# Kernel optimization log

Measured on AMD Instinct MI355X. Metric: run time of the kernel, lower is better.

Reference implementation:

```python
import jax, jax.numpy as jnp
import numpy as np

H = 384  # LSTM hidden size


def _conv1d(x, w, b, stride):
    # x: [B, T, Cin], w: [K, Cin, Cout] (flax 'SAME' padding, channels-last)
    y = jax.lax.conv_general_dilated(
        x, w, window_strides=(stride,), padding='SAME',
        dimension_numbers=('NWC', 'WIO', 'NWC'))
    return y + b


def _lstm(x, Wi, Wh, b, reverse):
    # x: [B, T, D]; Wi: [D, 4H] (input proj, no bias in flax LSTMCell input dense),
    # Wh: [H, 4H] (recurrent proj), b: [4H]. Gate order: i, f, g, o.
    if reverse:
        x = x[:, ::-1]
    B = x.shape[0]
    # precompute all input-to-gate projections in one big GEMM: [B, T, 4H]
    xg = jnp.einsum('btd,dh->bth', x, Wi)

    def step(carry, xg_t):
        c, h = carry
        z = xg_t + h @ Wh + b                      # [B, 4H]
        i, f, g, o = jnp.split(z, 4, axis=-1)
        i = jax.nn.sigmoid(i)
        f = jax.nn.sigmoid(f)
        g = jnp.tanh(g)
        o = jax.nn.sigmoid(o)
        c = f * c + i * g
        h = o * jnp.tanh(c)
        return (c, h), h

    init = (jnp.zeros((B, H), x.dtype), jnp.zeros((B, H), x.dtype))
    _, hs = jax.lax.scan(step, init, jnp.swapaxes(xg, 0, 1))  # hs: [T, B, H]
    hs = jnp.swapaxes(hs, 0, 1)
    if reverse:  # keep_order=True: flip output back to original time order
        hs = hs[:, ::-1]
    return hs


def setup_inputs() -> dict:
    key = jax.random.key(0)
    ks = jax.random.split(key, 12)
    s = 0.05
    B, T = 128, 8000
    return {
        'x': jax.random.normal(ks[0], (B, T, 1), jnp.float32),
        'conv1_w': jax.random.normal(ks[1], (5, 1, 4), jnp.float32) * s,
        'conv1_b': jnp.zeros((4,), jnp.float32),
        'conv2_w': jax.random.normal(ks[2], (5, 4, 16), jnp.float32) * s,
        'conv2_b': jnp.zeros((16,), jnp.float32),
        'conv3_w': jax.random.normal(ks[3], (19, 16, H), jnp.float32) * s,
        'conv3_b': jnp.zeros((H,), jnp.float32),
        'lstm_Wi': jax.random.normal(ks[4], (5, H, 4 * H), jnp.float32) * s,
        'lstm_Wh': jax.random.normal(ks[5], (5, H, 4 * H), jnp.float32) * s,
        'lstm_b': jnp.zeros((5, 4 * H), jnp.float32),
        'dense_w': jax.random.normal(ks[6], (H, 5), jnp.float32) * s,
        'dense_b': jnp.zeros((5,), jnp.float32),
    }


def reference(x, conv1_w, conv1_b, conv2_w, conv2_b, conv3_w, conv3_b,
              lstm_Wi, lstm_Wh, lstm_b, dense_w, dense_b):
    # CNN feature extractor
    x = jax.nn.silu(_conv1d(x, conv1_w, conv1_b, 1))
    x = jax.nn.silu(_conv1d(x, conv2_w, conv2_b, 1))
    x = jax.nn.silu(_conv1d(x, conv3_w, conv3_b, 5))   # [B, T/5, 384]
    # 5 stacked LSTMs, layers 1,3,5 reversed (keep_order), layers 2,4 forward
    for i in range(5):
        x = _lstm(x, lstm_Wi[i], lstm_Wh[i], lstm_b[i], reverse=(i % 2 == 0))
    # CTC head
    return x @ dense_w + dense_b                       # [B, T/5, 5]
```

## Files before the change

kernel.cpp:

```cpp
#include <hip/hip_runtime.h>
#include <math.h>

#define B_SZ 128
#define T_IN 8000
#define T_OUT 1600
#define HDIM 384
#define GDIM 1536
#define TC 40
#define NCHUNK (T_OUT / TC)
#define NTILES (12 * (B_SZ * TC / 128))
#define NLB 64

typedef _Float16 f16;
typedef __attribute__((ext_vector_type(2))) _Float16 f16x2;
typedef __attribute__((ext_vector_type(4))) _Float16 f16x4;
typedef __attribute__((ext_vector_type(8))) _Float16 f16x8;
typedef __attribute__((ext_vector_type(4))) float f32x4;
typedef __attribute__((ext_vector_type(4))) unsigned int u32x4;

__device__ inline float fdot2(f16x2 a, f16x2 b, float c) {
#if __has_builtin(__builtin_amdgcn_fdot2)
  return __builtin_amdgcn_fdot2(a, b, c, false);
#else
  return fmaf((float)a[0], (float)b[0], fmaf((float)a[1], (float)b[1], c));
#endif
}

__device__ inline float rcp_fast(float x) {
#if __has_builtin(__builtin_amdgcn_rcpf)
  return __builtin_amdgcn_rcpf(x);
#else
  return 1.f / x;
#endif
}
__device__ inline float sigf(float z) { return rcp_fast(1.f + __expf(-z)); }
__device__ inline float tanh_fast(float z) {
  z = fminf(fmaxf(z, -15.f), 15.f);
  float e = __expf(2.f * z);
  return (e - 1.f) * rcp_fast(e + 1.f);
}

__global__ __launch_bounds__(256) void conv12_kernel(
    const float* __restrict__ x, const float* __restrict__ w1, const float* __restrict__ b1,
    const float* __restrict__ w2, const float* __restrict__ b2, f16* __restrict__ y2) {
  __shared__ float sw1[20], sb1[4], sw2[320], sb2[16];
  int tid = threadIdx.x;
  if (tid < 20) sw1[tid] = w1[tid];
  if (tid < 4)  sb1[tid] = b1[tid];
  if (tid < 16) sb2[tid] = b2[tid];
  for (int i = tid; i < 320; i += 256) sw2[i] = w2[i];
  __syncthreads();
  int flat = blockIdx.x * 256 + tid;
  int b = flat / T_IN, t = flat % T_IN;
  const float* xb = x + (size_t)b * T_IN;
  float xv[9];
#pragma unroll
  for (int d = 0; d < 9; ++d) {
    int tt = t + d - 4;
    xv[d] = (tt >= 0 && tt < T_IN) ? xb[tt] : 0.f;
  }
  float y1[5][4];
#pragma unroll
  for (int u = 0; u < 5; ++u) {
    int tau = t + u - 2;
    bool valid = (tau >= 0 && tau < T_IN);
#pragma unroll
    for (int co = 0; co < 4; ++co) {
      float a = sb1[co];
#pragma unroll
      for (int k = 0; k < 5; ++k) a = fmaf(xv[u + k], sw1[k * 4 + co], a);
      y1[u][co] = valid ? (a / (1.f + expf(-a))) : 0.f;
    }
  }
  f16x8 o0, o1;
#pragma unroll
  for (int co = 0; co < 16; ++co) {
    float a = sb2[co];
#pragma unroll
    for (int u = 0; u < 5; ++u)
#pragma unroll
      for (int ci = 0; ci < 4; ++ci)
        a = fmaf(y1[u][ci], sw2[(u * 4 + ci) * 16 + co], a);
    float sv = a / (1.f + expf(-a));
    if (co < 8) o0[co] = (f16)sv; else o1[co - 8] = (f16)sv;
  }
  f16x8* dst = (f16x8*)(y2 + (size_t)flat * 16);
  dst[0] = o0;
  dst[1] = o1;
}

__global__ __launch_bounds__(384) void conv3_kernel(
    const f16* __restrict__ y2, const float* __restrict__ w3, const float* __restrict__ b3,
    f16* __restrict__ act) {
  __shared__ float in_s[94 * 16];
  int tid = threadIdx.x;
  int b = blockIdx.y;
  int t0 = blockIdx.x * 16;
  int base_t = t0 * 5 - 7;
  for (int i = tid; i < 94 * 16; i += 384) {
    int tau = i >> 4, ci = i & 15;
    int tt = base_t + tau;
    in_s[i] = (tt >= 0 && tt < T_IN) ? (float)y2[((size_t)b * T_IN + tt) * 16 + ci] : 0.f;
  }
  __syncthreads();
  int c = tid;
  float acc[16];
  float bv = b3[c];
#pragma unroll
  for (int tt = 0; tt < 16; ++tt) acc[tt] = bv;
  for (int kk = 0; kk < 19; ++kk) {
#pragma unroll
    for (int c4 = 0; c4 < 4; ++c4) {
      float wa = w3[(size_t)((kk * 16 + c4 * 4 + 0) * 384) + c];
      float wb = w3[(size_t)((kk * 16 + c4 * 4 + 1) * 384) + c];
      float wc = w3[(size_t)((kk * 16 + c4 * 4 + 2) * 384) + c];
      float wd = w3[(size_t)((kk * 16 + c4 * 4 + 3) * 384) + c];
#pragma unroll
      for (int tt = 0; tt < 16; ++tt) {
        const float4 iv = *(const float4*)&in_s[(tt * 5 + kk) * 16 + c4 * 4];
        acc[tt] = fmaf(iv.x, wa, acc[tt]);
        acc[tt] = fmaf(iv.y, wb, acc[tt]);
        acc[tt] = fmaf(iv.z, wc, acc[tt]);
        acc[tt] = fmaf(iv.w, wd, acc[tt]);
      }
    }
  }
#pragma unroll
  for (int tt = 0; tt < 16; ++tt) {
    float a = acc[tt];
    a = a / (1.f + expf(-a));
    act[((size_t)b * T_OUT + t0 + tt) * HDIM + c] = (f16)a;
  }
}

__global__ __launch_bounds__(256) void whcvt_kernel(
    const float* __restrict__ Wh, f16x2* __restrict__ whB) {
  size_t idx = (size_t)blockIdx.x * 256 + threadIdx.x;
  int d = (int)(idx & 3);
  size_t r1 = idx >> 2;
  int lane = (int)(r1 & 63);
  size_t r2 = r1 >> 6;
  int ks = (int)(r2 % 12);
  size_t r3 = r2 / 12;
  int nt = (int)(r3 % 12);
  size_t r4 = r3 / 12;
  int isl = (int)(r4 & 7);
  int L = (int)(r4 >> 3);
  int cz = nt * 16 + (lane & 15);
  int gate = cz & 3;
  int jj = cz >> 2;
  int gcol = gate * 384 + isl * 48 + jj;
  int k2d = ks * 16 + (lane >> 4) * 4 + d;
  const float* src = Wh + ((size_t)L * 384 + 2 * k2d) * 1536 + gcol;
  f16x2 v;
  v[0] = (f16)src[0];
  v[1] = (f16)src[1536];
  whB[idx] = v;
}

__global__ __launch_bounds__(256) void gemm_xg_kernel(
    const f16* __restrict__ act, const float* __restrict__ Bw,
    f16* __restrict__ C, int lo) {
  __shared__ f16x2 As2[8 * 136];
  __shared__ f16x2 Bs2[8 * 128];
  int tid = threadIdx.x;
  int n0 = blockIdx.x * 128;
  int m0 = blockIdx.y * 128;
  int am = tid >> 2;
  int ak = (tid & 3) * 4;
  int bk = tid >> 5;
  int bn = (tid & 31) * 4;
  int row0 = m0 + am, row1 = row0 + 64;
  const f16* Ap0 = act + ((size_t)(row0 / TC) * T_OUT + lo + row0 % TC) * HDIM + ak;
  const f16* Ap1 = act + ((size_t)(row1 / TC) * T_OUT + lo + row1 % TC) * HDIM + ak;
  const float* Bp = Bw + (size_t)(2 * bk) * GDIM + n0 + bn;
  f16x4 ra0 = *(const f16x4*)Ap0;
  f16x4 ra1 = *(const f16x4*)Ap1;
  float4 rb0 = *(const float4*)Bp;
  float4 rb1 = *(const float4*)(Bp + (size_t)GDIM);
  float acc[8][8];
#pragma unroll
  for (int i = 0; i < 8; ++i)
#pragma unroll
    for (int j = 0; j < 8; ++j) acc[i][j] = 0.f;
  int tx = tid & 15, ty = tid >> 4;
  for (int kt = 0; kt < 24; ++kt) {
    int ak2 = ak >> 1;
    As2[(ak2 + 0) * 136 + am] = (f16x2){ra0[0], ra0[1]};
    As2[(ak2 + 1) * 136 + am] = (f16x2){ra0[2], ra0[3]};
    As2[(ak2 + 0) * 136 + am + 64] = (f16x2){ra1[0], ra1[1]};
    As2[(ak2 + 1) * 136 + am + 64] = (f16x2){ra1[2], ra1[3]};
    Bs2[bk * 128 + bn + 0] = (f16x2){(f16)rb0.x, (f16)rb1.x};
    Bs2[bk * 128 + bn + 1] = (f16x2){(f16)rb0.y, (f16)rb1.y};
    Bs2[bk * 128 + bn + 2] = (f16x2){(f16)rb0.z, (f16)rb1.z};
    Bs2[bk * 128 + bn + 3] = (f16x2){(f16)rb0.w, (f16)rb1.w};
    __syncthreads();
    if (kt < 23) {
      Ap0 += 16; Ap1 += 16; Bp += (size_t)16 * GDIM;
      ra0 = *(const f16x4*)Ap0;
      ra1 = *(const f16x4*)Ap1;
      rb0 = *(const float4*)Bp;
      rb1 = *(const float4*)(Bp + (size_t)GDIM);
    }
#pragma unroll
    for (int k2 = 0; k2 < 8; ++k2) {
      f16x8 a0 = *(const f16x8*)&As2[k2 * 136 + ty * 4];
      f16x8 a1 = *(const f16x8*)&As2[k2 * 136 + 64 + ty * 4];
      f16x8 b0 = *(const f16x8*)&Bs2[k2 * 128 + tx * 4];
      f16x8 b1 = *(const f16x8*)&Bs2[k2 * 128 + 64 + tx * 4];
      f16x2 av[8], bv[8];
#pragma unroll
      for (int q = 0; q < 4; ++q) {
        av[q] = (f16x2){a0[2 * q], a0[2 * q + 1]};
        av[q + 4] = (f16x2){a1[2 * q], a1[2 * q + 1]};
        bv[q] = (f16x2){b0[2 * q], b0[2 * q + 1]};
        bv[q + 4] = (f16x2){b1[2 * q], b1[2 * q + 1]};
      }
#pragma unroll
      for (int i = 0; i < 8; ++i)
#pragma unroll
        for (int j = 0; j < 8; ++j) acc[i][j] = fdot2(av[i], bv[j], acc[i][j]);
    }
    __syncthreads();
  }
#pragma unroll
  for (int i = 0; i < 8; ++i) {
    int mi = (i < 4) ? (ty * 4 + i) : (64 + ty * 4 + i - 4);
    f16* Cp = C + (size_t)(m0 + mi) * GDIM + n0;
    f16x4 p0, p1;
    p0[0] = (f16)acc[i][0]; p0[1] = (f16)acc[i][1]; p0[2] = (f16)acc[i][2]; p0[3] = (f16)acc[i][3];
    p1[0] = (f16)acc[i][4]; p1[1] = (f16)acc[i][5]; p1[2] = (f16)acc[i][6]; p1[3] = (f16)acc[i][7];
    *(f16x4*)(Cp + tx * 4) = p0;
    *(f16x4*)(Cp + 64 + tx * 4) = p1;
  }
}

#define HSTR 784

union FusedSh {
  struct { char h2s[16 * HSTR]; unsigned pub[16 * 25]; } L;
  struct { f16x2 As2[3][8 * 136]; f16x2 Bs2[3][8 * 128]; } G;
  char pad[25600];
};

__global__ __launch_bounds__(768, 1) void fused_kernel(
    const f16* __restrict__ xgc_rd, f16* __restrict__ xgc_wr,
    const f16* __restrict__ whB, const float* __restrict__ bias,
    f16* __restrict__ act, float* __restrict__ cst, const float* __restrict__ Wi,
    unsigned* __restrict__ xh,
    int lo_l, int lo_g, int reverse, int first, int do_gemm, int epoch) {
  __shared__ FusedSh sh;
  int tid = threadIdx.x;

  if (blockIdx.x < NLB) {
    int wid = blockIdx.x;
    int g = wid & 7;
    int isl = wid >> 3;
    int b0 = g * 16;
    int nt = tid >> 6;
    int l = tid & 63;
    int bg = l >> 4;
    int qj = (l >> 2) & 3;
    int gate = l & 3;
    int jj = nt * 4 + qj;
    int hcol = isl * 48 + jj;
    int gcol = gate * 384 + isl * 48 + jj;

    f16x8 wreg[12];
    {
      const f16x8* wp = (const f16x8*)whB + (size_t)(isl * 12 + nt) * 12 * 64 + l;
#pragma unroll
      for (int ks = 0; ks < 12; ++ks) wreg[ks] = wp[(size_t)ks * 64];
#pragma unroll
      for (int ks = 0; ks < 12; ++ks) asm volatile("" : "+v"(wreg[ks]));
    }
    float bias_own = bias[gcol];

    float c_reg[4];
    if (first) {
#pragma unroll
      for (int r = 0; r < 4; ++r) c_reg[r] = 0.f;
      for (int i = tid; i < 16 * HSTR / 16; i += 768)
        *(f16x8*)(sh.L.h2s + i * 16) = (f16x8){};
    } else {
      int tprev = reverse ? (lo_l + TC) : (lo_l - 1);
#pragma unroll
      for (int r = 0; r < 4; ++r)
        c_reg[r] = cst[(size_t)(b0 + bg * 4 + r) * HDIM + hcol];
      int flat = tid * 8;
      int bt = flat / 384, c0 = flat % 384;
      *(f16x8*)(sh.L.h2s + bt * HSTR + c0 * 2) =
          *(const f16x8*)(act + ((size_t)(b0 + bt) * T_OUT + tprev) * HDIM + c0);
    }
    __syncthreads();

    const char* arow = sh.L.h2s + (l & 15) * HSTR + (l >> 4) * 16;
    unsigned short* pubh = (unsigned short*)sh.L.pub;

    int k2 = (tid % 3 == 0) ? (768 + tid / 3) : -1;

    float xv[4];
    {
      int tl0 = reverse ? (TC - 1) : 0;
      const f16* xb = xgc_rd + ((size_t)(b0 + bg * 4) * TC + tl0) * GDIM + gcol;
#pragma unroll
      for (int r = 0; r < 4; ++r) xv[r] = (float)xb[(size_t)r * TC * GDIM];
    }

    for (int s = 0; s < TC; ++s) {
      int t = reverse ? (lo_l + TC - 1 - s) : (lo_l + s);

      f32x4 acc = {0.f, 0.f, 0.f, 0.f};
#pragma unroll
      for (int ks = 0; ks < 12; ++ks) {
        f16x8 a = *(const f16x8*)(arow + ks * 64);
        acc = __builtin_amdgcn_mfma_f32_16x16x32_f16(a, wreg[ks], acc, 0, 0, 0);
      }

      f16 h16[4];
#pragma unroll
      for (int r = 0; r < 4; ++r) {
        float a = acc[r] + xv[r] + bias_own;
        float b = __shfl_xor(a, 1);
        float cc = __shfl_xor(a, 2);
        float dd = __shfl_xor(b, 2);
        float zi = (gate == 0) ? a : (gate == 1) ? b : (gate == 2) ? cc : dd;
        float zf = (gate == 1) ? a : (gate == 0) ? b : (gate == 3) ? cc : dd;
        float zg = (gate == 2) ? a : (gate == 3) ? b : (gate == 0) ? cc : dd;
        float zo = (gate == 3) ? a : (gate == 2) ? b : (gate == 1) ? cc : dd;
        float ig = sigf(zi), fg = sigf(zf), gv = tanh_fast(zg), og = sigf(zo);
        c_reg[r] = fg * c_reg[r] + ig * gv;
        h16[r] = (f16)(og * tanh_fast(c_reg[r]));
      }

      if (s + 1 < TC) {
        unsigned tag = (unsigned)(epoch * TC + s + 1);
        unsigned* slotbase = xh + (size_t)(s & 1) * 128 * 256;

        if (gate == 0) {
          int lcol = nt * 4 + qj;
#pragma unroll
          for (int r = 0; r < 4; ++r)
            pubh[(bg * 4 + r) * 50 + lcol] = __builtin_bit_cast(unsigned short, h16[r]);
        }
        __syncthreads();

        if (tid < 128) {
          int bt = tid >> 3, u = tid & 7;
          const unsigned* pw = sh.L.pub + bt * 25 + u * 3;
          u32x4 dnew;
          dnew[0] = pw[0]; dnew[1] = pw[1]; dnew[2] = pw[2]; dnew[3] = tag;
          u32x4* dp = (u32x4*)(slotbase + (((size_t)(b0 + bt) * 64) + isl * 8 + u) * 4);
          asm volatile("global_store_dwordx4 %0, %1, off sc0 sc1"
                       :: "v"(dp), "v"(dnew) : "memory");
        }

        if (gate == 0) {
#pragma unroll
          for (int r = 0; r < 4; ++r)
            act[((size_t)(b0 + bg * 4 + r) * T_OUT + t) * HDIM + hcol] = h16[r];
        }
        {
          int tl_n = reverse ? (TC - 2 - s) : (s + 1);
          const f16* xb = xgc_rd + ((size_t)(b0 + bg * 4) * TC + tl_n) * GDIM + gcol;
#pragma unroll
          for (int r = 0; r < 4; ++r) xv[r] = (float)xb[(size_t)r * TC * GDIM];
        }

        const u32x4* upA = nullptr; const u32x4* upB = nullptr;
        unsigned* dstA = nullptr; unsigned* dstB = nullptr;
#pragma unroll
        for (int uu = 0; uu < 2; ++uu) {
          int k = (uu == 0) ? tid : k2;
          if (uu == 1 && k < 0) break;
          int bt = k >> 6, rem = k & 63;
          int isl_src = rem >> 3, u = rem & 7;
          unsigned* dst = (unsigned*)(sh.L.h2s + bt * HSTR + isl_src * 96 + u * 12);
          if (isl_src == isl) {
            const unsigned* pw = sh.L.pub + bt * 25 + u * 3;
            dst[0] = pw[0]; dst[1] = pw[1]; dst[2] = pw[2];
          } else {
            const u32x4* up = (const u32x4*)(slotbase + (((size_t)(b0 + bt) * 64) + rem) * 4);
            if (!upA) { upA = up; dstA = dst; } else { upB = up; dstB = dst; }
          }
        }
        if (upA && !upB) {
          u32x4 v;
          while (true) {
            asm volatile("global_load_dwordx4 %0, %1, off sc0 sc1\n\ts_waitcnt vmcnt(0)"
                         : "=v"(v) : "v"(upA) : "memory");
            if (v[3] >= tag) break;
            __builtin_amdgcn_s_sleep(1);
          }
          dstA[0] = v[0]; dstA[1] = v[1]; dstA[2] = v[2];
        } else if (upA && upB) {
          u32x4 v0, v1;
          while (true) {
            asm volatile("global_load_dwordx4 %0, %2, off sc0 sc1\n\t"
                         "global_load_dwordx4 %1, %3, off sc0 sc1\n\t"
                         "s_waitcnt vmcnt(0)"
                         : "=&v"(v0), "=&v"(v1) : "v"(upA), "v"(upB) : "memory");
            if (v0[3] >= tag && v1[3] >= tag) break;
            __builtin_amdgcn_s_sleep(1);
          }
          dstA[0] = v0[0]; dstA[1] = v0[1]; dstA[2] = v0[2];
          dstB[0] = v1[0]; dstB[1] = v1[1]; dstB[2] = v1[2];
        }
        __syncthreads();
      } else {
        if (gate == 0) {
#pragma unroll
          for (int r = 0; r < 4; ++r)
            act[((size_t)(b0 + bg * 4 + r) * T_OUT + t) * HDIM + hcol] = h16[r];
        }
      }
    }
    if (gate == 0) {
#pragma unroll
      for (int r = 0; r < 4; ++r)
        cst[(size_t)(b0 + bg * 4 + r) * HDIM + hcol] = c_reg[r];
    }
  } else {
    if (!do_gemm) return;
    int wid = blockIdx.x - NLB;
    int sub = tid >> 8;
    int stid = tid & 255;
    int tileid = wid + 192 * sub;
    bool valid = (tileid < NTILES);
    int tclamp = valid ? tileid : 0;
    int n0 = (tclamp % 12) * 128;
    int m0 = (tclamp / 12) * 128;
    f16x2* As2 = &sh.G.As2[sub][0];
    f16x2* Bs2 = &sh.G.Bs2[sub][0];
    int am = stid >> 2;
    int ak = (stid & 3) * 4;
    int bk = stid >> 5;
    int bn = (stid & 31) * 4;
    int row0 = m0 + am, row1 = row0 + 64;
    const f16* Ap0 = act + ((size_t)(row0 / TC) * T_OUT + lo_g + row0 % TC) * HDIM + ak;
    const f16* Ap1 = act + ((size_t)(row1 / TC) * T_OUT + lo_g + row1 % TC) * HDIM + ak;
    const float* Bp = Wi + (size_t)(2 * bk) * GDIM + n0 + bn;
    f16x4 ra0 = {}, ra1 = {};
    float4 rb0 = {}, rb1 = {};
    if (valid) {
      ra0 = *(const f16x4*)Ap0;
      ra1 = *(const f16x4*)Ap1;
      rb0 = *(const float4*)Bp;
      rb1 = *(const float4*)(Bp + (size_t)GDIM);
    }
    float acc[8][8];
#pragma unroll
    for (int i = 0; i < 8; ++i)
#pragma unroll
      for (int j = 0; j < 8; ++j) acc[i][j] = 0.f;
    int tx = stid & 15, ty = stid >> 4;
    for (int kt = 0; kt < 24; ++kt) {
      if (valid) {
        int ak2 = ak >> 1;
        As2[(ak2 + 0) * 136 + am] = (f16x2){ra0[0], ra0[1]};
        As2[(ak2 + 1) * 136 + am] = (f16x2){ra0[2], ra0[3]};
        As2[(ak2 + 0) * 136 + am + 64] = (f16x2){ra1[0], ra1[1]};
        As2[(ak2 + 1) * 136 + am + 64] = (f16x2){ra1[2], ra1[3]};
        Bs2[bk * 128 + bn + 0] = (f16x2){(f16)rb0.x, (f16)rb1.x};
        Bs2[bk * 128 + bn + 1] = (f16x2){(f16)rb0.y, (f16)rb1.y};
        Bs2[bk * 128 + bn + 2] = (f16x2){(f16)rb0.z, (f16)rb1.z};
        Bs2[bk * 128 + bn + 3] = (f16x2){(f16)rb0.w, (f16)rb1.w};
      }
      __syncthreads();
      if (valid) {
        if (kt < 23) {
          Ap0 += 16; Ap1 += 16; Bp += (size_t)16 * GDIM;
          ra0 = *(const f16x4*)Ap0;
          ra1 = *(const f16x4*)Ap1;
          rb0 = *(const float4*)Bp;
          rb1 = *(const float4*)(Bp + (size_t)GDIM);
        }
#pragma unroll
        for (int k2i = 0; k2i < 8; ++k2i) {
          f16x8 a0 = *(const f16x8*)&As2[k2i * 136 + ty * 4];
          f16x8 a1 = *(const f16x8*)&As2[k2i * 136 + 64 + ty * 4];
          f16x8 b0 = *(const f16x8*)&Bs2[k2i * 128 + tx * 4];
          f16x8 b1 = *(const f16x8*)&Bs2[k2i * 128 + 64 + tx * 4];
          f16x2 av[8], bv[8];
#pragma unroll
          for (int qq = 0; qq < 4; ++qq) {
            av[qq] = (f16x2){a0[2 * qq], a0[2 * qq + 1]};
            av[qq + 4] = (f16x2){a1[2 * qq], a1[2 * qq + 1]};
            bv[qq] = (f16x2){b0[2 * qq], b0[2 * qq + 1]};
            bv[qq + 4] = (f16x2){b1[2 * qq], b1[2 * qq + 1]};
          }
#pragma unroll
          for (int i = 0; i < 8; ++i)
#pragma unroll
            for (int j = 0; j < 8; ++j) acc[i][j] = fdot2(av[i], bv[j], acc[i][j]);
        }
      }
      __syncthreads();
    }
    if (valid) {
#pragma unroll
      for (int i = 0; i < 8; ++i) {
        int mi = (i < 4) ? (ty * 4 + i) : (64 + ty * 4 + i - 4);
        f16* Cp = xgc_wr + (size_t)(m0 + mi) * GDIM + n0;
        f16x4 p0, p1;
        p0[0] = (f16)acc[i][0]; p0[1] = (f16)acc[i][1]; p0[2] = (f16)acc[i][2]; p0[3] = (f16)acc[i][3];
        p1[0] = (f16)acc[i][4]; p1[1] = (f16)acc[i][5]; p1[2] = (f16)acc[i][6]; p1[3] = (f16)acc[i][7];
        *(f16x4*)(Cp + tx * 4) = p0;
        *(f16x4*)(Cp + 64 + tx * 4) = p1;
      }
    }
  }
}

__global__ __launch_bounds__(256) void dense_kernel(
    const f16* __restrict__ h, const float* __restrict__ dw,
    const float* __restrict__ db, float* __restrict__ out) {
  __shared__ float ws_[1920];
  __shared__ float bs[5];
  int tid = threadIdx.x;
  for (int i = tid; i < 1920; i += 256) ws_[i] = dw[i];
  if (tid < 5) bs[tid] = db[tid];
  __syncthreads();
  size_t flat = (size_t)blockIdx.x * 256 + tid;
  const f16* hp = h + flat * HDIM;
  float acc[5];
#pragma unroll
  for (int o = 0; o < 5; ++o) acc[o] = bs[o];
  for (int d = 0; d < HDIM; d += 4) {
    f16x4 hv = *(const f16x4*)(hp + d);
#pragma unroll
    for (int o = 0; o < 5; ++o) {
      acc[o] = fmaf((float)hv[0], ws_[(d + 0) * 5 + o], acc[o]);
      acc[o] = fmaf((float)hv[1], ws_[(d + 1) * 5 + o], acc[o]);
      acc[o] = fmaf((float)hv[2], ws_[(d + 2) * 5 + o], acc[o]);
      acc[o] = fmaf((float)hv[3], ws_[(d + 3) * 5 + o], acc[o]);
    }
  }
  float* op = out + flat * 5;
#pragma unroll
  for (int o = 0; o < 5; ++o) op[o] = acc[o];
}

extern "C" void kernel_launch(void* const* d_in, const int* in_sizes, int n_in,
                              void* d_out, int out_size, void* d_ws, size_t ws_size,
                              hipStream_t stream) {
  const float* x  = (const float*)d_in[0];
  const float* w1 = (const float*)d_in[1];
  const float* b1 = (const float*)d_in[2];
  const float* w2 = (const float*)d_in[3];
  const float* b2 = (const float*)d_in[4];
  const float* w3 = (const float*)d_in[5];
  const float* b3 = (const float*)d_in[6];
  const float* Wi = (const float*)d_in[7];
  const float* Wh = (const float*)d_in[8];
  const float* lb = (const float*)d_in[9];
  const float* dw = (const float*)d_in[10];
  const float* db = (const float*)d_in[11];
  float* out = (float*)d_out;
  char* ws = (char*)d_ws;

  const size_t ACT_BYTES = (size_t)B_SZ * T_OUT * HDIM * 2;
  const size_t XGC_BYTES = (size_t)B_SZ * TC * GDIM * 2;
  const size_t WHB_BYTES = (size_t)5 * 8 * 12 * 12 * 64 * 16;
  const size_t CST_BYTES = (size_t)B_SZ * HDIM * 4;
  const size_t XH_BYTES  = (size_t)2 * 128 * 64 * 16;
  f16*      act  = (f16*)ws;
  f16*      xgcA = (f16*)(ws + ACT_BYTES);
  f16*      xgcB = (f16*)(ws + ACT_BYTES + XGC_BYTES);
  f16*      whB  = (f16*)(ws + ACT_BYTES + 2 * XGC_BYTES);
  float*    cst  = (float*)(ws + ACT_BYTES + 2 * XGC_BYTES + WHB_BYTES);
  unsigned* xh   = (unsigned*)(ws + ACT_BYTES + 2 * XGC_BYTES + WHB_BYTES + CST_BYTES);
  f16* y2 = xgcA;

  hipMemsetAsync(xh, 0, XH_BYTES, stream);

  hipLaunchKernelGGL(conv12_kernel, dim3(B_SZ * T_IN / 256), dim3(256), 0, stream,
                     x, w1, b1, w2, b2, y2);
  hipLaunchKernelGGL(conv3_kernel, dim3(T_OUT / 16, B_SZ), dim3(384), 0, stream,
                     y2, w3, b3, act);
  hipLaunchKernelGGL(whcvt_kernel, dim3((unsigned)(WHB_BYTES / 4 / 256)), dim3(256), 0, stream,
                     Wh, (f16x2*)whB);

  for (int l = 0; l < 5; ++l) {
    int rev = (l % 2 == 0) ? 1 : 0;
    const float* wi_p = Wi + (size_t)l * HDIM * GDIM;
    const f16* wh_p = whB + (size_t)l * 8 * 12 * 12 * 64 * 8;
    const float* lb_p = lb + (size_t)l * GDIM;
    int lo0 = rev ? (T_OUT - TC) : 0;
    hipLaunchKernelGGL(gemm_xg_kernel, dim3(GDIM / 128, (B_SZ * TC) / 128), dim3(256), 0, stream,
                       act, wi_p, xgcA, lo0);
    for (int ci = 0; ci < NCHUNK; ++ci) {
      int lo_l = rev ? (T_OUT - (ci + 1) * TC) : (ci * TC);
      int do_gemm = (ci + 1 < NCHUNK) ? 1 : 0;
      int lo_g = do_gemm ? (rev ? (T_OUT - (ci + 2) * TC) : ((ci + 1) * TC)) : 0;
      f16* rd = (ci % 2 == 0) ? xgcA : xgcB;
      f16* wr = (ci % 2 == 0) ? xgcB : xgcA;
      int epoch = l * NCHUNK + ci;
      hipLaunchKernelGGL(fused_kernel, dim3(256), dim3(768), 0, stream,
                         rd, wr, wh_p, lb_p, act, cst, wi_p, xh,
                         lo_l, lo_g, rev, (ci == 0) ? 1 : 0, do_gemm, epoch);
    }
  }
  hipLaunchKernelGGL(dense_kernel, dim3((B_SZ * T_OUT) / 256), dim3(256), 0, stream,
                     act, dw, db, out);
}
```

Measured before the change: 27.73 ms.

## Move conv3 to MFMA and add a fast-path mailbox for cross-block h exchange

Conv3 now runs as an fp16 MFMA GEMM over an im2col-style shared tile, using a pre-transposed, zero-padded fp16 weight copy, in place of scalar fp32 FMAs. Separately, the LSTM cross-block hidden-state exchange writes each slot to two buffers. One buffer takes stores and loads with sc0 only (narrower coherence scope), the other keeps system-scope sc0 sc1; pollers read the fast buffer first and fall back to the slow one after 24 retries. This aims to cut synchronisation latency on the recurrent critical path. The risks are reduced conv3 precision, and stale or invisible data in the fast buffer if sc0 alone does not give cross-CU visibility, which the fallback is there to cover.

```diff
diff --git a/kernel.cpp b/kernel.cpp
--- a/kernel.cpp
+++ b/kernel.cpp
@@ -89,48 +89,77 @@
   dst[1] = o1;
 }
 
+__global__ __launch_bounds__(256) void w3cvt_kernel(
+    const float* __restrict__ w3, f16* __restrict__ w3t) {
+  int idx = blockIdx.x * 256 + threadIdx.x;
+  int c = idx / 320, k = idx - c * 320;
+  w3t[idx] = (k < 304) ? (f16)w3[(size_t)k * 384 + c] : (f16)0.f;
+}
+
+#define C3M 32
+#define C3K 320
+#define INSP 24
+#define BSTP 40
+
 __global__ __launch_bounds__(384) void conv3_kernel(
-    const f16* __restrict__ y2, const float* __restrict__ w3, const float* __restrict__ b3,
-    f16* __restrict__ act) {
-  __shared__ float in_s[94 * 16];
+    const f16* __restrict__ y2, const f16* __restrict__ w3t,
+    const float* __restrict__ b3, f16* __restrict__ act) {
+  __shared__ f16 in_s[176 * INSP];
+  __shared__ f16 bs_t[384 * BSTP];
   int tid = threadIdx.x;
   int b = blockIdx.y;
-  int t0 = blockIdx.x * 16;
+  int t0 = blockIdx.x * C3M;
   int base_t = t0 * 5 - 7;
-  for (int i = tid; i < 94 * 16; i += 384) {
-    int tau = i >> 4, ci = i & 15;
+  for (int j = tid; j < 352; j += 384) {
+    int tau = j >> 1, ci0 = (j & 1) * 8;
     int tt = base_t + tau;
-    in_s[i] = (tt >= 0 && tt < T_IN) ? (float)y2[((size_t)b * T_IN + tt) * 16 + ci] : 0.f;
-  }
-  __syncthreads();
-  int c = tid;
-  float acc[16];
-  float bv = b3[c];
-#pragma unroll
-  for (int tt = 0; tt < 16; ++tt) acc[tt] = bv;
-  for (int kk = 0; kk < 19; ++kk) {
-#pragma unroll
-    for (int c4 = 0; c4 < 4; ++c4) {
-      float wa = w3[(size_t)((kk * 16 + c4 * 4 + 0) * 384) + c];
-      float wb = w3[(size_t)((kk * 16 + c4 * 4 + 1) * 384) + c];
-      float wc = w3[(size_t)((kk * 16 + c4 * 4 + 2) * 384) + c];
-      float wd = w3[(size_t)((kk * 16 + c4 * 4 + 3) * 384) + c];
-#pragma unroll
-      for (int tt = 0; tt < 16; ++tt) {
-        const float4 iv = *(const float4*)&in_s[(tt * 5 + kk) * 16 + c4 * 4];
-        acc[tt] = fmaf(iv.x, wa, acc[tt]);
-        acc[tt] = fmaf(iv.y, wb, acc[tt]);
-        acc[tt] = fmaf(iv.z, wc, acc[tt]);
-        acc[tt] = fmaf(iv.w, wd, acc[tt]);
-      }
-    }
-  }
-#pragma unroll
-  for (int tt = 0; tt < 16; ++tt) {
-    float a = acc[tt];
-    a = a / (1.f + expf(-a));
-    act[((size_t)b * T_OUT + t0 + tt) * HDIM + c] = (f16)a;
-  }
+    f16x8 v = {};
+    if (tt >= 0 && tt < T_IN)
+      v = *(const f16x8*)(y2 + ((size_t)b * T_IN + tt) * 16 + ci0);
+    *(f16x8*)&in_s[tau * INSP + ci0] = v;
+  }
+  int wv = tid >> 6;
+  int l = tid & 63;
+  int lm = l & 15;
+  int lk = l >> 4;
+  f32x4 acc[2][4];
+#pragma unroll
+  for (int mt = 0; mt < 2; ++mt)
+#pragma unroll
+    for (int q = 0; q < 4; ++q) acc[mt][q] = (f32x4){0.f, 0.f, 0.f, 0.f};
+  for (int ks = 0; ks < 10; ++ks) {
+    __syncthreads();
+    for (int u = tid; u < 1536; u += 384) {
+      int c = u >> 2, k8 = u & 3;
+      *(f16x8*)&bs_t[c * BSTP + k8 * 8] =
+          *(const f16x8*)(w3t + (size_t)c * C3K + ks * 32 + k8 * 8);
+    }
+    __syncthreads();
+    int kg = ks * 32 + lk * 8;
+    int kk = kg >> 4, ci = kg & 15;
+    f16x8 a0 = *(const f16x8*)&in_s[(lm * 5 + kk) * INSP + ci];
+    f16x8 a1 = *(const f16x8*)&in_s[((lm + 16) * 5 + kk) * INSP + ci];
+#pragma unroll
+    for (int q = 0; q < 4; ++q) {
+      f16x8 bf = *(const f16x8*)&bs_t[((wv * 4 + q) * 16 + lm) * BSTP + lk * 8];
+      acc[0][q] = __builtin_amdgcn_mfma_f32_16x16x32_f16(a0, bf, acc[0][q], 0, 0, 0);
+      acc[1][q] = __builtin_amdgcn_mfma_f32_16x16x32_f16(a1, bf, acc[1][q], 0, 0, 0);
+    }
+  }
+#pragma unroll
+  for (int mt = 0; mt < 2; ++mt)
+#pragma unroll
+    for (int q = 0; q < 4; ++q) {
+      int n = (wv * 4 + q) * 16 + lm;
+      float bv = b3[n];
+#pragma unroll
+      for (int r = 0; r < 4; ++r) {
+        int m = mt * 16 + lk * 4 + r;
+        float a = acc[mt][q][r] + bv;
+        a = a / (1.f + expf(-a));
+        act[((size_t)b * T_OUT + t0 + m) * HDIM + n] = (f16)a;
+      }
+    }
 }
 
 __global__ __launch_bounds__(256) void whcvt_kernel(
@@ -247,7 +276,7 @@
     const f16* __restrict__ xgc_rd, f16* __restrict__ xgc_wr,
     const f16* __restrict__ whB, const float* __restrict__ bias,
     f16* __restrict__ act, float* __restrict__ cst, const float* __restrict__ Wi,
-    unsigned* __restrict__ xh,
+    unsigned* __restrict__ xhS, unsigned* __restrict__ xhF,
     int lo_l, int lo_g, int reverse, int first, int do_gemm, int epoch) {
   __shared__ FusedSh sh;
   int tid = threadIdx.x;
@@ -335,7 +364,9 @@
 
       if (s + 1 < TC) {
         unsigned tag = (unsigned)(epoch * TC + s + 1);
-        unsigned* slotbase = xh + (size_t)(s & 1) * 128 * 256;
+        size_t parity = (size_t)(s & 1) * 128 * 256;
+        unsigned* slowbase = xhS + parity;
+        unsigned* fastbase = xhF + parity;
 
         if (gate == 0) {
           int lcol = nt * 4 + qj;
@@ -350,9 +381,12 @@
           const unsigned* pw = sh.L.pub + bt * 25 + u * 3;
           u32x4 dnew;
           dnew[0] = pw[0]; dnew[1] = pw[1]; dnew[2] = pw[2]; dnew[3] = tag;
-          u32x4* dp = (u32x4*)(slotbase + (((size_t)(b0 + bt) * 64) + isl * 8 + u) * 4);
-          asm volatile("global_store_dwordx4 %0, %1, off sc0 sc1"
-                       :: "v"(dp), "v"(dnew) : "memory");
+          size_t off = (((size_t)(b0 + bt) * 64) + isl * 8 + u) * 4;
+          u32x4* dpF = (u32x4*)(fastbase + off);
+          u32x4* dpS = (u32x4*)(slowbase + off);
+          asm volatile("global_store_dwordx4 %0, %2, off sc0\n\t"
+                       "global_store_dwordx4 %1, %2, off sc0 sc1"
+                       :: "v"(dpF), "v"(dpS), "v"(dnew) : "memory");
         }
 
         if (gate == 0) {
@@ -367,7 +401,8 @@
           for (int r = 0; r < 4; ++r) xv[r] = (float)xb[(size_t)r * TC * GDIM];
         }
 
-        const u32x4* upA = nullptr; const u32x4* upB = nullptr;
+        const u32x4* fA = nullptr; const u32x4* fB = nullptr;
+        const u32x4* sA = nullptr; const u32x4* sB = nullptr;
         unsigned* dstA = nullptr; unsigned* dstB = nullptr;
 #pragma unroll
         for (int uu = 0; uu < 2; ++uu) {
@@ -380,27 +415,47 @@
             const unsigned* pw = sh.L.pub + bt * 25 + u * 3;
             dst[0] = pw[0]; dst[1] = pw[1]; dst[2] = pw[2];
           } else {
-            const u32x4* up = (const u32x4*)(slotbase + (((size_t)(b0 + bt) * 64) + rem) * 4);
-            if (!upA) { upA = up; dstA = dst; } else { upB = up; dstB = dst; }
+            size_t off = (((size_t)(b0 + bt) * 64) + rem) * 4;
+            if (!fA) {
+              fA = (const u32x4*)(fastbase + off);
+              sA = (const u32x4*)(slowbase + off);
+              dstA = dst;
+            } else {
+              fB = (const u32x4*)(fastbase + off);
+              sB = (const u32x4*)(slowbase + off);
+              dstB = dst;
+            }
           }
         }
-        if (upA && !upB) {
-          u32x4 v;
+        if (fA && !fB) {
+          u32x4 v; int tr = 0;
           while (true) {
-            asm volatile("global_load_dwordx4 %0, %1, off sc0 sc1\n\ts_waitcnt vmcnt(0)"
-                         : "=v"(v) : "v"(upA) : "memory");
+            if (tr < 24)
+              asm volatile("global_load_dwordx4 %0, %1, off sc0\n\ts_waitcnt vmcnt(0)"
+                           : "=v"(v) : "v"(fA) : "memory");
+            else
+              asm volatile("global_load_dwordx4 %0, %1, off sc0 sc1\n\ts_waitcnt vmcnt(0)"
+                           : "=v"(v) : "v"(sA) : "memory");
             if (v[3] >= tag) break;
+            ++tr;
             __builtin_amdgcn_s_sleep(1);
           }
           dstA[0] = v[0]; dstA[1] = v[1]; dstA[2] = v[2];
-        } else if (upA && upB) {
-          u32x4 v0, v1;
+        } else if (fA && fB) {
+          u32x4 v0, v1; int tr = 0;
           while (true) {
-            asm volatile("global_load_dwordx4 %0, %2, off sc0 sc1\n\t"
-                         "global_load_dwordx4 %1, %3, off sc0 sc1\n\t"
-                         "s_waitcnt vmcnt(0)"
-                         : "=&v"(v0), "=&v"(v1) : "v"(upA), "v"(upB) : "memory");
+            if (tr < 24)
+              asm volatile("global_load_dwordx4 %0, %2, off sc0\n\t"
+                           "global_load_dwordx4 %1, %3, off sc0\n\t"
+                           "s_waitcnt vmcnt(0)"
+                           : "=&v"(v0), "=&v"(v1) : "v"(fA), "v"(fB) : "memory");
+            else
+              asm volatile("global_load_dwordx4 %0, %2, off sc0 sc1\n\t"
+                           "global_load_dwordx4 %1, %3, off sc0 sc1\n\t"
+                           "s_waitcnt vmcnt(0)"
+                           : "=&v"(v0), "=&v"(v1) : "v"(sA), "v"(sB) : "memory");
             if (v0[3] >= tag && v1[3] >= tag) break;
+            ++tr;
             __builtin_amdgcn_s_sleep(1);
           }
           dstA[0] = v0[0]; dstA[1] = v0[1]; dstA[2] = v0[2];
@@ -564,20 +619,25 @@
   const size_t WHB_BYTES = (size_t)5 * 8 * 12 * 12 * 64 * 16;
   const size_t CST_BYTES = (size_t)B_SZ * HDIM * 4;
   const size_t XH_BYTES  = (size_t)2 * 128 * 64 * 16;
+  const size_t W3T_BYTES = (size_t)384 * 320 * 2;
   f16*      act  = (f16*)ws;
   f16*      xgcA = (f16*)(ws + ACT_BYTES);
   f16*      xgcB = (f16*)(ws + ACT_BYTES + XGC_BYTES);
   f16*      whB  = (f16*)(ws + ACT_BYTES + 2 * XGC_BYTES);
   float*    cst  = (float*)(ws + ACT_BYTES + 2 * XGC_BYTES + WHB_BYTES);
-  unsigned* xh   = (unsigned*)(ws + ACT_BYTES + 2 * XGC_BYTES + WHB_BYTES + CST_BYTES);
+  unsigned* xhS  = (unsigned*)(ws + ACT_BYTES + 2 * XGC_BYTES + WHB_BYTES + CST_BYTES);
+  unsigned* xhF  = (unsigned*)(ws + ACT_BYTES + 2 * XGC_BYTES + WHB_BYTES + CST_BYTES + XH_BYTES);
+  f16*      w3t  = (f16*)(ws + ACT_BYTES + 2 * XGC_BYTES + WHB_BYTES + CST_BYTES + 2 * XH_BYTES);
   f16* y2 = xgcA;
 
-  hipMemsetAsync(xh, 0, XH_BYTES, stream);
+  hipMemsetAsync(xhS, 0, 2 * XH_BYTES, stream);
 
   hipLaunchKernelGGL(conv12_kernel, dim3(B_SZ * T_IN / 256), dim3(256), 0, stream,
                      x, w1, b1, w2, b2, y2);
-  hipLaunchKernelGGL(conv3_kernel, dim3(T_OUT / 16, B_SZ), dim3(384), 0, stream,
-                     y2, w3, b3, act);
+  hipLaunchKernelGGL(w3cvt_kernel, dim3(384 * 320 / 256), dim3(256), 0, stream,
+                     w3, w3t);
+  hipLaunchKernelGGL(conv3_kernel, dim3(T_OUT / C3M, B_SZ), dim3(384), 0, stream,
+                     y2, w3t, b3, act);
   hipLaunchKernelGGL(whcvt_kernel, dim3((unsigned)(WHB_BYTES / 4 / 256)), dim3(256), 0, stream,
                      Wh, (f16x2*)whB);
 
@@ -597,7 +657,7 @@
       f16* wr = (ci % 2 == 0) ? xgcB : xgcA;
       int epoch = l * NCHUNK + ci;
       hipLaunchKernelGGL(fused_kernel, dim3(256), dim3(768), 0, stream,
-                         rd, wr, wh_p, lb_p, act, cst, wi_p, xh,
+                         rd, wr, wh_p, lb_p, act, cst, wi_p, xhS, xhF,
                          lo_l, lo_g, rev, (ci == 0) ? 1 : 0, do_gemm, epoch);
     }
   }
```

Result: slower. 59.48 ms (+114.5%).
